# Optimization experiments

Measured on AMD Instinct MI355X. Metric: run time of the kernel, lower is better.

## Reference

```python
import jax, jax.numpy as jnp
import numpy as np

H = 16  # head_num
NEG = -1000000.0


def setup_inputs() -> dict:
    key = jax.random.key(0)
    k1, k2, k3 = jax.random.split(key, 3)
    B, S, D = 4, 2048, 1024
    d = D // H
    x = jax.random.normal(k1, (B, S, D), dtype=jnp.float32)
    mask = jax.random.randint(k2, (B, S), 0, 2, dtype=jnp.int32)
    W = jax.random.normal(k3, (d, d), dtype=jnp.float32) * (1.0 / np.sqrt(d))
    b = jnp.zeros((d,), dtype=jnp.float32)
    return {"x": x, "mask": mask, "W": W, "b": b}


def reference(x, mask, W, b):
    B, S, D = x.shape
    d = D // H
    # [B,S,D] -> [B,H,S,d]
    x_h = jnp.transpose(x.reshape(B, S, H, d), (0, 2, 1, 3))
    # shared Dense(d) produces q and k (and the unused v) with the SAME weights
    q = x_h @ W + b
    k = x_h @ W + b
    # scores, scaled by d (not sqrt(d)) as in the source
    qkt = jnp.einsum('bhqd,bhkd->bhqk', q, k) / d
    # additive mask: (1-mask)*-1e6, broadcast [B,1,S,1] over query rows
    m = (1.0 - mask.astype(x.dtype)) * NEG
    qkt = qkt + m[:, None, :, None]
    attn = jax.nn.softmax(qkt, axis=-1)
    # second matmul uses x_h (not v), per the source
    a = jnp.einsum('bhqk,bhkd->bhqd', attn, x_h)
    # direct reshape (no head transpose back), per the source
    return a.reshape(B, S, D)
```

## Files before the change

### kernel.cpp

```cpp
#include <hip/hip_runtime.h>
#include <math.h>


#define S_LEN   2048
#define D_MODEL 1024
#define HD      64
#define NHEAD   16
#define QT      128
#define QW      32
#define KT2     64
#define NKT     (S_LEN / KT2)
#define PH_STRIDE 36
#define PH_BUF  (QT * PH_STRIDE)

typedef __bf16 bf16;
typedef __bf16 bf16x8 __attribute__((ext_vector_type(8)));
typedef __bf16 bf16x4 __attribute__((ext_vector_type(4)));
typedef __bf16 bf16x2 __attribute__((ext_vector_type(2)));
typedef float  floatx4 __attribute__((ext_vector_type(4)));
typedef unsigned int u32;
typedef u32 u32x4 __attribute__((ext_vector_type(4)));

#define SCALE 0.02254211001389005324f

__device__ __forceinline__ floatx4 mfma16(bf16x8 a, bf16x8 b, floatx4 c) {
    return __builtin_amdgcn_mfma_f32_16x16x32_bf16(a, b, c, 0, 0, 0);
}

__device__ __forceinline__ void ldsdma16(void* lds_base, const void* gsrc) {
    __builtin_amdgcn_global_load_lds(
        (const __attribute__((address_space(1))) u32*)gsrc,
        (__attribute__((address_space(3))) u32*)lds_base, 16, 0, 0);
}

__device__ __forceinline__ u32 pack2(bf16 lo, bf16 hi) {
    bf16x2 p = { lo, hi };
    return __builtin_bit_cast(u32, p);
}

__global__ __launch_bounds__(256)
void prex_kernel(const float* __restrict__ x, const float* __restrict__ W,
                 const float* __restrict__ bvec,
                 bf16* __restrict__ Xb, bf16* __restrict__ XT,
                 float* __restrict__ Uout, bf16* __restrict__ Mout) {
    __shared__ __align__(16) char smem[16896];
    u32*   sT = (u32*)smem;
    float* Wp = (float*)smem;
    float* bs = (float*)(smem + 16640);

    const int tid = threadIdx.x;
    const int st = blockIdx.x, h = blockIdx.y, b = blockIdx.z;

    if (st == 16) {
        if (h != 0 || b != 0) return;
        for (int i = tid; i < 4096; i += 256) Wp[(i >> 6) * 65 + (i & 63)] = W[i];
        if (tid < 64) bs[tid] = bvec[tid];
        __syncthreads();
        for (int e = tid; e < 4096; e += 256) {
            int i = e >> 6, j = e & 63;
            float acc = 0.f;
            #pragma unroll 8
            for (int c = 0; c < 64; ++c) acc += Wp[i * 65 + c] * Wp[j * 65 + c];
            Mout[e] = (bf16)(acc * SCALE);
        }
        if (tid < 64) {
            float acc = 0.f;
            #pragma unroll 8
            for (int c = 0; c < 64; ++c) acc += Wp[tid * 65 + c] * bs[c];
            Uout[tid] = acc * SCALE;
        }
        return;
    }

    const int bh = b * NHEAD + h;
    const float* xbh = x + (size_t)b * S_LEN * D_MODEL + (size_t)st * 128 * D_MODEL + h * HD;
    bf16* Xbbh = Xb + ((size_t)bh * S_LEN + st * 128) * HD;

    const int t  = tid & 15;
    const int rp = tid >> 4;
    const int c4 = t * 4;

    #pragma unroll
    for (int it = 0; it < 4; ++it) {
        const int r0 = it * 32 + rp * 2;
        float4 v0 = *(const float4*)(xbh + (size_t)r0 * D_MODEL + c4);
        float4 v1 = *(const float4*)(xbh + (size_t)(r0 + 1) * D_MODEL + c4);
        bf16 a0 = (bf16)v0.x, a1 = (bf16)v0.y, a2 = (bf16)v0.z, a3 = (bf16)v0.w;
        bf16 b0 = (bf16)v1.x, b1 = (bf16)v1.y, b2 = (bf16)v1.z, b3 = (bf16)v1.w;
        bf16x4 p0 = { a0, a1, a2, a3 }, p1 = { b0, b1, b2, b3 };
        *(bf16x4*)(Xbbh + (size_t)r0 * HD + c4)       = p0;
        *(bf16x4*)(Xbbh + (size_t)(r0 + 1) * HD + c4) = p1;
        const int w = it * 16 + rp;
        sT[(c4 + 0) * 65 + w] = pack2(a0, b0);
        sT[(c4 + 1) * 65 + w] = pack2(a1, b1);
        sT[(c4 + 2) * 65 + w] = pack2(a2, b2);
        sT[(c4 + 3) * 65 + w] = pack2(a3, b3);
    }
    __syncthreads();

    bf16* XTbh = XT + (size_t)bh * HD * S_LEN + (size_t)st * 128;
    #pragma unroll
    for (int i = 0; i < 4; ++i) {
        const int c  = i * 256 + tid;
        const int dd = c >> 4;
        const int wg = (c & 15) * 4;
        u32x4 qv = { sT[dd * 65 + wg],     sT[dd * 65 + wg + 1],
                     sT[dd * 65 + wg + 2], sT[dd * 65 + wg + 3] };
        *(u32x4*)((char*)(XTbh + (size_t)dd * S_LEN) + (size_t)wg * 4) = qv;
    }
}

__global__ __launch_bounds__(256, 3)
void attn_kernel(const bf16* __restrict__ Xb, const bf16* __restrict__ XT,
                 const bf16* __restrict__ Mw, const float* __restrict__ Uv,
                 float* __restrict__ out) {
    __shared__ bf16 sXk [2 * KT2 * HD];
    __shared__ bf16 sXkT[2 * HD * KT2];
    __shared__ bf16 sP  [2 * PH_BUF];

    const int tid  = threadIdx.x;
    const int wave = tid >> 6, lane = tid & 63;
    const int quad = lane >> 4, low = lane & 15;
    const int wbase = wave * QW;
    const int bh = blockIdx.x, qt = blockIdx.y;
    const int q0 = qt * QT;

    const char* Xbh  = (const char*)(Xb + (size_t)bh * S_LEN * HD);
    const char* XTbh = (const char*)(XT + (size_t)bh * HD * S_LEN);

    floatx4 zero4 = {0.f, 0.f, 0.f, 0.f};
    bf16x8 Tfrag[2][2];
    {
        float uS[4];
        #pragma unroll
        for (int nt = 0; nt < 4; ++nt) uS[nt] = Uv[nt * 16 + low];

        floatx4 Tacc[2][4];
        #pragma unroll
        for (int mt = 0; mt < 2; ++mt)
            #pragma unroll
            for (int nt = 0; nt < 4; ++nt) Tacc[mt][nt] = zero4;
        #pragma unroll
        for (int kc = 0; kc < 2; ++kc) {
            bf16x8 aq[2];
            #pragma unroll
            for (int mt = 0; mt < 2; ++mt)
                aq[mt] = *(const bf16x8*)(Xbh +
                    (size_t)(q0 + wbase + mt * 16 + low) * 128 + kc * 64 + quad * 16);
            #pragma unroll
            for (int nt = 0; nt < 4; ++nt) {
                bf16x8 bm = *(const bf16x8*)(Mw + (nt * 16 + low) * 64 + kc * 32 + quad * 8);
                #pragma unroll
                for (int mt = 0; mt < 2; ++mt)
                    Tacc[mt][nt] = mfma16(aq[mt], bm, Tacc[mt][nt]);
            }
        }
        #pragma unroll
        for (int mt = 0; mt < 2; ++mt)
            #pragma unroll
            for (int nt = 0; nt < 4; ++nt)
                #pragma unroll
                for (int r = 0; r < 4; ++r) Tacc[mt][nt][r] += uS[nt];

        #pragma unroll
        for (int p = 0; p < 2; ++p) {
            bf16* sPp = sP + p * PH_BUF;
            #pragma unroll
            for (int mt = 0; mt < 2; ++mt)
                #pragma unroll
                for (int ntl = 0; ntl < 2; ++ntl)
                    #pragma unroll
                    for (int r = 0; r < 4; ++r)
                        sPp[(wbase + mt * 16 + quad * 4 + r) * PH_STRIDE + ntl * 16 + low] =
                            (bf16)Tacc[mt][p * 2 + ntl][r];
            #pragma unroll
            for (int mt = 0; mt < 2; ++mt) {
                const bf16* pp = &sPp[(wbase + mt * 16 + low) * PH_STRIDE + quad * 8];
                bf16x4 al = *(const bf16x4*)pp, ah = *(const bf16x4*)(pp + 4);
                Tfrag[mt][p] = __builtin_shufflevector(al, ah, 0, 1, 2, 3, 4, 5, 6, 7);
            }
        }
    }

    auto stage = [&](int kt, int par) {
        const int k0 = kt * KT2;
        #pragma unroll
        for (int j = 0; j < 2; ++j) {
            int s = wave * 16 + j * 8 + (lane >> 3);
            const char* g = Xbh + (size_t)(k0 + s) * 128 + (((lane & 7) ^ (s & 7)) << 4);
            ldsdma16((char*)sXk + par * 8192 + (wave * 16 + j * 8) * 128, g);
        }
        #pragma unroll
        for (int j = 0; j < 2; ++j) {
            int dd = wave * 16 + j * 8 + (lane >> 3);
            const char* g = XTbh + (size_t)dd * 4096 + (size_t)k0 * 2 + (((lane & 7) ^ (dd & 7)) << 4);
            ldsdma16((char*)sXkT + par * 8192 + (wave * 16 + j * 8) * 128, g);
        }
    };

    floatx4 Oacc[2][4];
    float l_run[2][4];
    #pragma unroll
    for (int mt = 0; mt < 2; ++mt) {
        #pragma unroll
        for (int nt = 0; nt < 4; ++nt) Oacc[mt][nt] = zero4;
        #pragma unroll
        for (int r = 0; r < 4; ++r) l_run[mt][r] = 0.f;
    }

    stage(0, 0);

    auto body = [&](int kt, const int par) {
        __syncthreads();
        if (kt + 1 < NKT) stage(kt + 1, par ^ 1);

        const char* xkb = (const char*)sXk + par * 8192;
        floatx4 Sacc[2][4];
        #pragma unroll
        for (int mt = 0; mt < 2; ++mt)
            #pragma unroll
            for (int nt = 0; nt < 4; ++nt) Sacc[mt][nt] = zero4;
        __builtin_amdgcn_s_setprio(1);
        #pragma unroll
        for (int kc = 0; kc < 2; ++kc)
            #pragma unroll
            for (int nt = 0; nt < 4; ++nt) {
                int row = nt * 16 + low;
                bf16x8 bk = *(const bf16x8*)(
                    xkb + row * 128 + ((((kc << 2) + quad) ^ (low & 7)) << 4));
                #pragma unroll
                for (int mt = 0; mt < 2; ++mt)
                    Sacc[mt][nt] = mfma16(Tfrag[mt][kc], bk, Sacc[mt][nt]);
            }
        __builtin_amdgcn_s_setprio(0);

        const char* xktb = (const char*)sXkT + par * 8192;
        #pragma unroll
        for (int p = 0; p < 2; ++p) {
            bf16* sPp = sP + p * PH_BUF;
            #pragma unroll
            for (int mt = 0; mt < 2; ++mt)
                #pragma unroll
                for (int ntl = 0; ntl < 2; ++ntl)
                    #pragma unroll
                    for (int r = 0; r < 4; ++r) {
                        float pe = __builtin_amdgcn_exp2f(Sacc[mt][p * 2 + ntl][r]);
                        l_run[mt][r] += pe;
                        sPp[(wbase + mt * 16 + quad * 4 + r) * PH_STRIDE + ntl * 16 + low] =
                            (bf16)pe;
                    }
        }
        #pragma unroll
        for (int p = 0; p < 2; ++p) {
            const bf16* sPp = sP + p * PH_BUF;
            bf16x8 pa[2];
            #pragma unroll
            for (int mt = 0; mt < 2; ++mt) {
                const bf16* pp = &sPp[(wbase + mt * 16 + low) * PH_STRIDE + quad * 8];
                bf16x4 al = *(const bf16x4*)pp, ah = *(const bf16x4*)(pp + 4);
                pa[mt] = __builtin_shufflevector(al, ah, 0, 1, 2, 3, 4, 5, 6, 7);
            }
            __builtin_amdgcn_s_setprio(1);
            #pragma unroll
            for (int nt = 0; nt < 4; ++nt) {
                int row = nt * 16 + low;
                bf16x8 bb = *(const bf16x8*)(
                    xktb + row * 128 + ((((p << 2) + quad) ^ (low & 7)) << 4));
                #pragma unroll
                for (int mt = 0; mt < 2; ++mt)
                    Oacc[mt][nt] = mfma16(pa[mt], bb, Oacc[mt][nt]);
            }
            __builtin_amdgcn_s_setprio(0);
        }
    };

    for (int kt = 0; kt < NKT; kt += 2) {
        body(kt, 0);
        body(kt + 1, 1);
    }

    float* outb = out + ((size_t)bh * S_LEN + q0) * HD;
    #pragma unroll
    for (int mt = 0; mt < 2; ++mt)
        #pragma unroll
        for (int r = 0; r < 4; ++r) {
            float l = l_run[mt][r];
            l += __shfl_xor(l, 1);
            l += __shfl_xor(l, 2);
            l += __shfl_xor(l, 4);
            l += __shfl_xor(l, 8);
            float rl = 1.0f / l;
            int qrow = wbase + mt * 16 + quad * 4 + r;
            #pragma unroll
            for (int nt = 0; nt < 4; ++nt)
                outb[(size_t)qrow * HD + nt * 16 + low] = Oacc[mt][nt][r] * rl;
        }
}

extern "C" void kernel_launch(void* const* d_in, const int* in_sizes, int n_in,
                              void* d_out, int out_size, void* d_ws, size_t ws_size,
                              hipStream_t stream) {
    const float* x    = (const float*)d_in[0];
    const float* W    = (const float*)d_in[2];
    const float* bvec = (const float*)d_in[3];

    bf16*  Mws = (bf16*)d_ws;
    float* Uws = (float*)((char*)d_ws + 8192);
    bf16*  Xbws = (bf16*)((char*)d_ws + 540672);
    bf16*  XTws = (bf16*)((char*)d_ws + 17317888);

    prex_kernel<<<dim3(17, 16, 4), dim3(256), 0, stream>>>(x, W, bvec,
                                                           Xbws, XTws, Uws, Mws);
    attn_kernel<<<dim3(64, 16, 1), dim3(256), 0, stream>>>(Xbws, XTws, Mws, Uws,
                                                           (float*)d_out);
}
```

Before: 204.2 us.

## Switch attention to 32x32x16 MFMA with register-resident P via permlane swaps

Rewrites the attention kernel to use 32x32x16 bf16 MFMA tiles, with each wave covering 64 query rows and 256-row query tiles per block. The LDS round-trip for the T fragments and softmax probabilities is dropped. Their bf16 operand fragments are now built in registers using v_cvt_pk_bf16_f32 and v_permlane32_swap. This reduces LDS traffic and reuses each K/X tile over twice as many queries. In exchange, register pressure rises, occupancy falls to 2 blocks per CU, and the grid halves to 512 blocks.

```diff
diff --git a/kernel.cpp b/kernel.cpp
--- a/kernel.cpp
+++ b/kernel.cpp
@@ -6,25 +6,22 @@
 #define D_MODEL 1024
 #define HD      64
 #define NHEAD   16
-#define QT      128
-#define QW      32
+#define QT      256
 #define KT2     64
 #define NKT     (S_LEN / KT2)
-#define PH_STRIDE 36
-#define PH_BUF  (QT * PH_STRIDE)
 
 typedef __bf16 bf16;
 typedef __bf16 bf16x8 __attribute__((ext_vector_type(8)));
 typedef __bf16 bf16x4 __attribute__((ext_vector_type(4)));
 typedef __bf16 bf16x2 __attribute__((ext_vector_type(2)));
-typedef float  floatx4 __attribute__((ext_vector_type(4)));
+typedef float  floatx16 __attribute__((ext_vector_type(16)));
 typedef unsigned int u32;
 typedef u32 u32x4 __attribute__((ext_vector_type(4)));
 
 #define SCALE 0.02254211001389005324f
 
-__device__ __forceinline__ floatx4 mfma16(bf16x8 a, bf16x8 b, floatx4 c) {
-    return __builtin_amdgcn_mfma_f32_16x16x32_bf16(a, b, c, 0, 0, 0);
+__device__ __forceinline__ floatx16 mfma32(bf16x8 a, bf16x8 b, floatx16 c) {
+    return __builtin_amdgcn_mfma_f32_32x32x16_bf16(a, b, c, 0, 0, 0);
 }
 
 __device__ __forceinline__ void ldsdma16(void* lds_base, const void* gsrc) {
@@ -36,6 +33,15 @@
 __device__ __forceinline__ u32 pack2(bf16 lo, bf16 hi) {
     bf16x2 p = { lo, hi };
     return __builtin_bit_cast(u32, p);
+}
+
+__device__ __forceinline__ u32 cvtpk(float lo, float hi) {
+    u32 r;
+    asm("v_cvt_pk_bf16_f32 %0, %1, %2" : "=v"(r) : "v"(lo), "v"(hi));
+    return r;
+}
+__device__ __forceinline__ void swap32(u32& x, u32& y) {
+    asm("v_permlane32_swap_b32 %0, %1" : "+v"(x), "+v"(y));
 }
 
 __global__ __launch_bounds__(256)
@@ -110,76 +116,72 @@
     }
 }
 
-__global__ __launch_bounds__(256, 3)
+__global__ __launch_bounds__(256, 2)
 void attn_kernel(const bf16* __restrict__ Xb, const bf16* __restrict__ XT,
                  const bf16* __restrict__ Mw, const float* __restrict__ Uv,
                  float* __restrict__ out) {
-    __shared__ bf16 sXk [2 * KT2 * HD];
-    __shared__ bf16 sXkT[2 * HD * KT2];
-    __shared__ bf16 sP  [2 * PH_BUF];
+    __shared__ bf16  sXk [2 * KT2 * HD];
+    __shared__ bf16  sXkT[2 * HD * KT2];
+    __shared__ float sL[4][64];
 
     const int tid  = threadIdx.x;
     const int wave = tid >> 6, lane = tid & 63;
-    const int quad = lane >> 4, low = lane & 15;
-    const int wbase = wave * QW;
+    const int hi   = lane >> 5, q32 = lane & 31;
+    const int wbase = wave * 64;
     const int bh = blockIdx.x, qt = blockIdx.y;
     const int q0 = qt * QT;
 
     const char* Xbh  = (const char*)(Xb + (size_t)bh * S_LEN * HD);
     const char* XTbh = (const char*)(XT + (size_t)bh * HD * S_LEN);
 
-    floatx4 zero4 = {0.f, 0.f, 0.f, 0.f};
-    bf16x8 Tfrag[2][2];
+    const floatx16 z16 = {0,0,0,0, 0,0,0,0, 0,0,0,0, 0,0,0,0};
+
+    bf16x8 Tfrag[2][4];
     {
-        float uS[4];
-        #pragma unroll
-        for (int nt = 0; nt < 4; ++nt) uS[nt] = Uv[nt * 16 + low];
-
-        floatx4 Tacc[2][4];
+        floatx16 Tacc[2][2];
         #pragma unroll
         for (int mt = 0; mt < 2; ++mt)
             #pragma unroll
-            for (int nt = 0; nt < 4; ++nt) Tacc[mt][nt] = zero4;
-        #pragma unroll
-        for (int kc = 0; kc < 2; ++kc) {
-            bf16x8 aq[2];
+            for (int ddt = 0; ddt < 2; ++ddt) Tacc[mt][ddt] = z16;
+
+        #pragma unroll
+        for (int kc = 0; kc < 4; ++kc) {
+            bf16x8 am[2], xq[2];
+            #pragma unroll
+            for (int ddt = 0; ddt < 2; ++ddt)
+                am[ddt] = *(const bf16x8*)(Mw + (ddt * 32 + q32) * 64 + kc * 16 + hi * 8);
             #pragma unroll
             for (int mt = 0; mt < 2; ++mt)
-                aq[mt] = *(const bf16x8*)(Xbh +
-                    (size_t)(q0 + wbase + mt * 16 + low) * 128 + kc * 64 + quad * 16);
-            #pragma unroll
-            for (int nt = 0; nt < 4; ++nt) {
-                bf16x8 bm = *(const bf16x8*)(Mw + (nt * 16 + low) * 64 + kc * 32 + quad * 8);
-                #pragma unroll
-                for (int mt = 0; mt < 2; ++mt)
-                    Tacc[mt][nt] = mfma16(aq[mt], bm, Tacc[mt][nt]);
+                xq[mt] = *(const bf16x8*)(Xbh +
+                    (size_t)(q0 + wbase + mt * 32 + q32) * 128 + kc * 32 + hi * 16);
+            #pragma unroll
+            for (int mt = 0; mt < 2; ++mt)
+                #pragma unroll
+                for (int ddt = 0; ddt < 2; ++ddt)
+                    Tacc[mt][ddt] = mfma32(am[ddt], xq[mt], Tacc[mt][ddt]);
+        }
+        #pragma unroll
+        for (int ddt = 0; ddt < 2; ++ddt)
+            #pragma unroll
+            for (int r = 0; r < 16; ++r) {
+                float uu = Uv[ddt * 32 + 8 * (r >> 2) + 4 * hi + (r & 3)];
+                #pragma unroll
+                for (int mt = 0; mt < 2; ++mt) Tacc[mt][ddt][r] += uu;
             }
-        }
         #pragma unroll
         for (int mt = 0; mt < 2; ++mt)
             #pragma unroll
-            for (int nt = 0; nt < 4; ++nt)
-                #pragma unroll
-                for (int r = 0; r < 4; ++r) Tacc[mt][nt][r] += uS[nt];
-
-        #pragma unroll
-        for (int p = 0; p < 2; ++p) {
-            bf16* sPp = sP + p * PH_BUF;
-            #pragma unroll
-            for (int mt = 0; mt < 2; ++mt)
-                #pragma unroll
-                for (int ntl = 0; ntl < 2; ++ntl)
-                    #pragma unroll
-                    for (int r = 0; r < 4; ++r)
-                        sPp[(wbase + mt * 16 + quad * 4 + r) * PH_STRIDE + ntl * 16 + low] =
-                            (bf16)Tacc[mt][p * 2 + ntl][r];
-            #pragma unroll
-            for (int mt = 0; mt < 2; ++mt) {
-                const bf16* pp = &sPp[(wbase + mt * 16 + low) * PH_STRIDE + quad * 8];
-                bf16x4 al = *(const bf16x4*)pp, ah = *(const bf16x4*)(pp + 4);
-                Tfrag[mt][p] = __builtin_shufflevector(al, ah, 0, 1, 2, 3, 4, 5, 6, 7);
+            for (int kc = 0; kc < 4; ++kc) {
+                const int ddt = kc >> 1, a4 = 8 * (kc & 1);
+                u32 X  = cvtpk(Tacc[mt][ddt][a4 + 0], Tacc[mt][ddt][a4 + 1]);
+                u32 Y  = cvtpk(Tacc[mt][ddt][a4 + 4], Tacc[mt][ddt][a4 + 5]);
+                swap32(X, Y);
+                u32 X2 = cvtpk(Tacc[mt][ddt][a4 + 2], Tacc[mt][ddt][a4 + 3]);
+                u32 Y2 = cvtpk(Tacc[mt][ddt][a4 + 6], Tacc[mt][ddt][a4 + 7]);
+                swap32(X2, Y2);
+                u32x4 w = { X, X2, Y, Y2 };
+                Tfrag[mt][kc] = __builtin_bit_cast(bf16x8, w);
             }
-        }
     }
 
     auto stage = [&](int kt, int par) {
@@ -198,15 +200,12 @@
         }
     };
 
-    floatx4 Oacc[2][4];
-    float l_run[2][4];
-    #pragma unroll
-    for (int mt = 0; mt < 2; ++mt) {
-        #pragma unroll
-        for (int nt = 0; nt < 4; ++nt) Oacc[mt][nt] = zero4;
-        #pragma unroll
-        for (int r = 0; r < 4; ++r) l_run[mt][r] = 0.f;
-    }
+    floatx16 Oacc[2][2];
+    float l_run[2] = {0.f, 0.f};
+    #pragma unroll
+    for (int mt = 0; mt < 2; ++mt)
+        #pragma unroll
+        for (int nt = 0; nt < 2; ++nt) Oacc[mt][nt] = z16;
 
     stage(0, 0);
 
@@ -215,60 +214,63 @@
         if (kt + 1 < NKT) stage(kt + 1, par ^ 1);
 
         const char* xkb = (const char*)sXk + par * 8192;
-        floatx4 Sacc[2][4];
+        floatx16 Sacc[2][2];
         #pragma unroll
         for (int mt = 0; mt < 2; ++mt)
             #pragma unroll
-            for (int nt = 0; nt < 4; ++nt) Sacc[mt][nt] = zero4;
+            for (int k32t = 0; k32t < 2; ++k32t) Sacc[mt][k32t] = z16;
         __builtin_amdgcn_s_setprio(1);
         #pragma unroll
-        for (int kc = 0; kc < 2; ++kc)
-            #pragma unroll
-            for (int nt = 0; nt < 4; ++nt) {
-                int row = nt * 16 + low;
-                bf16x8 bk = *(const bf16x8*)(
-                    xkb + row * 128 + ((((kc << 2) + quad) ^ (low & 7)) << 4));
-                #pragma unroll
-                for (int mt = 0; mt < 2; ++mt)
-                    Sacc[mt][nt] = mfma16(Tfrag[mt][kc], bk, Sacc[mt][nt]);
-            }
+        for (int kc = 0; kc < 4; ++kc) {
+            bf16x8 ak[2];
+            #pragma unroll
+            for (int k32t = 0; k32t < 2; ++k32t)
+                ak[k32t] = *(const bf16x8*)(xkb + (k32t * 32 + q32) * 128 +
+                                            (((2 * kc + hi) ^ (q32 & 7)) << 4));
+            #pragma unroll
+            for (int mt = 0; mt < 2; ++mt)
+                #pragma unroll
+                for (int k32t = 0; k32t < 2; ++k32t)
+                    Sacc[mt][k32t] = mfma32(ak[k32t], Tfrag[mt][kc], Sacc[mt][k32t]);
+        }
         __builtin_amdgcn_s_setprio(0);
 
+        #pragma unroll
+        for (int mt = 0; mt < 2; ++mt)
+            #pragma unroll
+            for (int k32t = 0; k32t < 2; ++k32t)
+                #pragma unroll
+                for (int r = 0; r < 16; ++r) {
+                    float pe = __builtin_amdgcn_exp2f(Sacc[mt][k32t][r]);
+                    Sacc[mt][k32t][r] = pe;
+                    l_run[mt] += pe;
+                }
+
         const char* xktb = (const char*)sXkT + par * 8192;
         #pragma unroll
-        for (int p = 0; p < 2; ++p) {
-            bf16* sPp = sP + p * PH_BUF;
-            #pragma unroll
-            for (int mt = 0; mt < 2; ++mt)
-                #pragma unroll
-                for (int ntl = 0; ntl < 2; ++ntl)
-                    #pragma unroll
-                    for (int r = 0; r < 4; ++r) {
-                        float pe = __builtin_amdgcn_exp2f(Sacc[mt][p * 2 + ntl][r]);
-                        l_run[mt][r] += pe;
-                        sPp[(wbase + mt * 16 + quad * 4 + r) * PH_STRIDE + ntl * 16 + low] =
-                            (bf16)pe;
-                    }
-        }
-        #pragma unroll
-        for (int p = 0; p < 2; ++p) {
-            const bf16* sPp = sP + p * PH_BUF;
+        for (int s = 0; s < 4; ++s) {
+            const int k32t = s >> 1, a4 = 8 * (s & 1);
             bf16x8 pa[2];
             #pragma unroll
             for (int mt = 0; mt < 2; ++mt) {
-                const bf16* pp = &sPp[(wbase + mt * 16 + low) * PH_STRIDE + quad * 8];
-                bf16x4 al = *(const bf16x4*)pp, ah = *(const bf16x4*)(pp + 4);
-                pa[mt] = __builtin_shufflevector(al, ah, 0, 1, 2, 3, 4, 5, 6, 7);
+                u32 X  = cvtpk(Sacc[mt][k32t][a4 + 0], Sacc[mt][k32t][a4 + 1]);
+                u32 Y  = cvtpk(Sacc[mt][k32t][a4 + 4], Sacc[mt][k32t][a4 + 5]);
+                swap32(X, Y);
+                u32 X2 = cvtpk(Sacc[mt][k32t][a4 + 2], Sacc[mt][k32t][a4 + 3]);
+                u32 Y2 = cvtpk(Sacc[mt][k32t][a4 + 6], Sacc[mt][k32t][a4 + 7]);
+                swap32(X2, Y2);
+                u32x4 w = { X, X2, Y, Y2 };
+                pa[mt] = __builtin_bit_cast(bf16x8, w);
             }
             __builtin_amdgcn_s_setprio(1);
             #pragma unroll
-            for (int nt = 0; nt < 4; ++nt) {
-                int row = nt * 16 + low;
-                bf16x8 bb = *(const bf16x8*)(
-                    xktb + row * 128 + ((((p << 2) + quad) ^ (low & 7)) << 4));
+            for (int nt = 0; nt < 2; ++nt) {
+                const int dd = nt * 32 + q32;
+                bf16x8 bb = *(const bf16x8*)(xktb + dd * 128 +
+                                             (((2 * s + hi) ^ (q32 & 7)) << 4));
                 #pragma unroll
                 for (int mt = 0; mt < 2; ++mt)
-                    Oacc[mt][nt] = mfma16(pa[mt], bb, Oacc[mt][nt]);
+                    Oacc[mt][nt] = mfma32(pa[mt], bb, Oacc[mt][nt]);
             }
             __builtin_amdgcn_s_setprio(0);
         }
@@ -279,21 +281,24 @@
         body(kt + 1, 1);
     }
 
+    #pragma unroll
+    for (int mt = 0; mt < 2; ++mt) {
+        float lt = l_run[mt] + __shfl_xor(l_run[mt], 32);
+        if (hi == 0) sL[wave][mt * 32 + q32] = 1.0f / lt;
+    }
+    __syncthreads();
+
     float* outb = out + ((size_t)bh * S_LEN + q0) * HD;
     #pragma unroll
     for (int mt = 0; mt < 2; ++mt)
         #pragma unroll
-        for (int r = 0; r < 4; ++r) {
-            float l = l_run[mt][r];
-            l += __shfl_xor(l, 1);
-            l += __shfl_xor(l, 2);
-            l += __shfl_xor(l, 4);
-            l += __shfl_xor(l, 8);
-            float rl = 1.0f / l;
-            int qrow = wbase + mt * 16 + quad * 4 + r;
-            #pragma unroll
-            for (int nt = 0; nt < 4; ++nt)
-                outb[(size_t)qrow * HD + nt * 16 + low] = Oacc[mt][nt][r] * rl;
+        for (int r = 0; r < 16; ++r) {
+            const int qlocal = 8 * (r >> 2) + 4 * hi + (r & 3);
+            const float rl = sL[wave][mt * 32 + qlocal];
+            const int qrow = wbase + mt * 32 + qlocal;
+            #pragma unroll
+            for (int nt = 0; nt < 2; ++nt)
+                outb[(size_t)qrow * HD + nt * 32 + q32] = Oacc[mt][nt][r] * rl;
         }
 }
 
@@ -311,6 +316,6 @@
 
     prex_kernel<<<dim3(17, 16, 4), dim3(256), 0, stream>>>(x, W, bvec,
                                                            Xbws, XTws, Uws, Mws);
-    attn_kernel<<<dim3(64, 16, 1), dim3(256), 0, stream>>>(Xbws, XTws, Mws, Uws,
+    attn_kernel<<<dim3(64, 8, 1),  dim3(256), 0, stream>>>(Xbws, XTws, Mws, Uws,
                                                            (float*)d_out);
 }
```

Measured after the change: 167.0 us. -18.2%, faster.
